# Optimization experiments

Hardware: AMD Instinct MI355X
Metric: run time of the kernel (lower is better)

The kernel has to match this reference:

```python
import jax, jax.numpy as jnp
import numpy as np

N, M = 1024, 1024
GATES = ["ii", "hi", "if", "hf", "ig", "hg", "io", "ho"]


def setup_inputs() -> dict:
    key = jax.random.key(0)
    names = ["x", "h", "c"] + [f"{p}_{g}" for g in GATES for p in ("L", "R", "b")]
    keys = jax.random.split(key, len(names))
    out = {}
    for nm, k in zip(names, keys):
        if nm in ("x", "h", "c"):
            sh = (N, M)
            scale = 1.0
        else:
            p = nm.split("_")[0]
            sh = {"L": (N, N), "R": (M, M), "b": (N, M)}[p]
            scale = 0.05  # keep gate pre-activations in a sane range
        out[nm] = jax.random.normal(k, sh, dtype=jnp.float32) * scale
    return out


def _klin(L, R, b, x):
    # kronecker_addmm: left @ x @ right + bias
    return L @ x @ R + b


def reference(x, h, c,
              L_ii, R_ii, b_ii, L_hi, R_hi, b_hi,
              L_if, R_if, b_if, L_hf, R_hf, b_hf,
              L_ig, R_ig, b_ig, L_hg, R_hg, b_hg,
              L_io, R_io, b_io, L_ho, R_ho, b_ho):
    i = jax.nn.sigmoid(_klin(L_ii, R_ii, b_ii, x) + _klin(L_hi, R_hi, b_hi, h))
    f = jax.nn.sigmoid(_klin(L_if, R_if, b_if, x) + _klin(L_hf, R_hf, b_hf, h))
    g = jnp.tanh(_klin(L_ig, R_ig, b_ig, x) + _klin(L_hg, R_hg, b_hg, h))
    o = jax.nn.sigmoid(_klin(L_io, R_io, b_io, x) + _klin(L_ho, R_ho, b_ho, h))
    c_new = f * c + i * g
    h_new = o * jnp.tanh(c_new)
    return (h_new, c_new)
```

## Files before the change

kernel.cpp:

```cpp
#include <hip/hip_runtime.h>
#include <stdint.h>

typedef __bf16 bf16x8 __attribute__((ext_vector_type(8)));
typedef float  f32x4  __attribute__((ext_vector_type(4)));
typedef uint16_t u16;

#define MAT_ELEMS (1024 * 1024)
#define LDK 1024


__device__ __forceinline__ u16 to_bf16(float f) {
  union { float f; uint32_t u; } v; v.f = f;
  uint32_t u = v.u;
  uint32_t r = u + 0x7FFFu + ((u >> 16) & 1u);
  return (u16)(r >> 16);
}

__device__ __forceinline__ float bf16_to_f32(u16 b) {
  union { uint32_t u; float f; } v; v.u = ((uint32_t)b) << 16;
  return v.f;
}

__device__ __forceinline__ void gll16(const void* g, void* l) {
  __builtin_amdgcn_global_load_lds(
      (__attribute__((address_space(1))) void*)const_cast<void*>(g),
      (__attribute__((address_space(3))) void*)(l),
      16, 0, 0);
}

__device__ __forceinline__ void wait_barrier() {
  asm volatile("s_waitcnt vmcnt(0)" ::: "memory");
  __builtin_amdgcn_s_barrier();
  __builtin_amdgcn_sched_barrier(0);
}

__device__ __forceinline__ float fast_sigmoid(float x) {
  x = fminf(fmaxf(x, -30.f), 30.f);
  return 1.0f / (1.0f + __expf(-x));
}

__device__ __forceinline__ float fast_tanh(float x) {
  x = fminf(fmaxf(x, -15.f), 15.f);
  float e = __expf(2.0f * x);
  return (e - 1.0f) / (e + 1.0f);
}


struct P8  { const float* p[8]; };
struct P10 { const float* p[10]; };
struct B8  { const float* b[8]; };

__global__ __launch_bounds__(256) void cast8_kernel(P8 s, u16* __restrict__ dst) {
  const float* src = s.p[blockIdx.y];
  u16* d = dst + ((size_t)blockIdx.y << 20);
  int i = (blockIdx.x * 256 + threadIdx.x) * 4;
  f32x4 v = *reinterpret_cast<const f32x4*>(src + i);
  ushort4 o;
  o.x = to_bf16(v[0]); o.y = to_bf16(v[1]);
  o.z = to_bf16(v[2]); o.w = to_bf16(v[3]);
  *reinterpret_cast<ushort4*>(d + i) = o;
}

__global__ __launch_bounds__(256) void transpose_cast_kernel(P10 s, u16* __restrict__ dstbase) {
  __shared__ float tile[32][65];
  const float* src = s.p[blockIdx.z];
  u16* dst = dstbase + ((size_t)blockIdx.z << 20);
  int c0 = blockIdx.x * 64;
  int r0 = blockIdx.y * 32;
  int cl = threadIdx.x & 63;
  int rg = threadIdx.x >> 6;
#pragma unroll
  for (int i = 0; i < 8; ++i) {
    int r = rg + i * 4;
    tile[r][cl] = src[(size_t)(r0 + r) * 1024 + c0 + cl];
  }
  __syncthreads();
  int kl = threadIdx.x & 31;
  int ng = threadIdx.x >> 5;
#pragma unroll
  for (int i = 0; i < 8; ++i) {
    int n = ng + i * 8;
    dst[(size_t)(c0 + n) * 1024 + r0 + kl] = to_bf16(tile[kl][n]);
  }
}


struct GemmCtx {
  const u16* A; const u16* B;
  int row0, col0;
  int tid, wr, wc, r16, kg, sw;
};

__device__ __forceinline__ void stage_tile(const GemmCtx& c, u16* As, u16* Bs, int kt) {
  int rho = c.tid >> 2;
  int sig = c.tid & 3;
  int swc = (sig ^ ((c.tid >> 3) & 3)) * 8;
  int kcol = kt * 32 + swc;
  gll16(c.A + (size_t)(c.row0 + rho) * LDK + kcol, As + c.tid * 8);
  gll16(c.B + (size_t)(c.col0 + rho) * LDK + kcol, Bs + c.tid * 8);
  gll16(c.B + (size_t)(c.col0 + rho + 128) * LDK + kcol, Bs + c.tid * 8 + 4096);
}

__device__ __forceinline__ void compute_tile(const GemmCtx& c, const u16* As,
                                             const u16* Bs, f32x4 acc[4][4]) {
  bf16x8 af[4], bfr[4];
#pragma unroll
  for (int n = 0; n < 4; ++n) {
    int Rb = c.wc * 64 + n * 16 + c.r16;
    bfr[n] = *reinterpret_cast<const bf16x8*>(Bs + Rb * 32 + ((c.kg ^ c.sw) * 8));
  }
#pragma unroll
  for (int m = 0; m < 4; ++m) {
    int Ra = c.wr * 64 + m * 16 + c.r16;
    af[m] = *reinterpret_cast<const bf16x8*>(As + Ra * 32 + ((c.kg ^ c.sw) * 8));
  }
#pragma unroll
  for (int m = 0; m < 4; ++m)
#pragma unroll
    for (int n = 0; n < 4; ++n)
      acc[m][n] = __builtin_amdgcn_mfma_f32_16x16x32_bf16(af[m], bfr[n], acc[m][n], 0, 0, 0);
}

__device__ __forceinline__ void gemm_body(
    const u16* __restrict__ A, const u16* __restrict__ B,
    int row0, int col0, u16* __restrict__ out,
    u16* As0, u16* Bs0, u16* As1, u16* Bs1)
{
  GemmCtx c;
  c.A = A; c.B = B; c.row0 = row0; c.col0 = col0;
  c.tid = threadIdx.x;
  int lane = c.tid & 63;
  int w = c.tid >> 6;
  c.wr  = w >> 2;
  c.wc  = w & 3;
  c.r16 = lane & 15;
  c.kg  = lane >> 4;
  c.sw  = (c.r16 >> 1) & 3;

  f32x4 acc[4][4];
#pragma unroll
  for (int m = 0; m < 4; ++m)
#pragma unroll
    for (int n = 0; n < 4; ++n) {
      f32x4 z = {0.f, 0.f, 0.f, 0.f};
      acc[m][n] = z;
    }

  stage_tile(c, As0, Bs0, 0);
  wait_barrier();

  for (int kt = 0; kt < 32; kt += 2) {
    stage_tile(c, As1, Bs1, kt + 1);
    compute_tile(c, As0, Bs0, acc);
    wait_barrier();
    if (kt + 2 < 32) stage_tile(c, As0, Bs0, kt + 2);
    compute_tile(c, As1, Bs1, acc);
    wait_barrier();
  }

#pragma unroll
  for (int m = 0; m < 4; ++m) {
#pragma unroll
    for (int r = 0; r < 4; ++r) {
      int row = row0 + c.wr * 64 + m * 16 + c.kg * 4 + r;
#pragma unroll
      for (int n = 0; n < 4; ++n) {
        int col = col0 + c.wc * 64 + n * 16 + c.r16;
        out[(size_t)row * 1024 + col] = to_bf16(acc[m][n][r]);
      }
    }
  }
}

__device__ __forceinline__ void swz_decode(int bx, int& g, int& row0, int& col0) {
  int wg = ((bx & 7) << 5) | (bx >> 3);
  g = wg >> 5;
  int t = wg & 31;
  row0 = (t >> 2) * 128;
  col0 = (t & 3) * 256;
}

__global__ __launch_bounds__(512) void gemm_stage1_kernel(
    const u16* __restrict__ Lb, const u16* __restrict__ xT,
    const u16* __restrict__ hT, u16* __restrict__ Tbuf)
{
  __shared__ u16 As0[128 * 32], Bs0[256 * 32];
  __shared__ u16 As1[128 * 32], Bs1[256 * 32];
  int g, row0, col0;
  swz_decode(blockIdx.x, g, row0, col0);
  const u16* A = Lb + ((size_t)g << 20);
  const u16* B = (g & 1) ? hT : xT;
  gemm_body(A, B, row0, col0, Tbuf + ((size_t)g << 20), As0, Bs0, As1, Bs1);
}

__global__ __launch_bounds__(512) void gemm_stage2_kernel(
    const u16* __restrict__ Tbuf, const u16* __restrict__ RT,
    u16* __restrict__ P)
{
  __shared__ u16 As0[128 * 32], Bs0[256 * 32];
  __shared__ u16 As1[128 * 32], Bs1[256 * 32];
  int g, row0, col0;
  swz_decode(blockIdx.x, g, row0, col0);
  const u16* A = Tbuf + ((size_t)g << 20);
  const u16* B = RT   + ((size_t)g << 20);
  gemm_body(A, B, row0, col0, P + ((size_t)g << 20), As0, Bs0, As1, Bs1);
}

__global__ __launch_bounds__(256) void lstm_cell_kernel(
    const u16* __restrict__ P, B8 bp, const float* __restrict__ c,
    float* __restrict__ out)
{
  int i = (blockIdx.x * 256 + threadIdx.x) * 4;
  ushort4 pv[8];
#pragma unroll
  for (int g = 0; g < 8; ++g)
    pv[g] = *reinterpret_cast<const ushort4*>(P + (size_t)g * MAT_ELEMS + i);
  f32x4 bv[8];
#pragma unroll
  for (int g = 0; g < 8; ++g)
    bv[g] = *reinterpret_cast<const f32x4*>(bp.b[g] + i);
  f32x4 cc = *reinterpret_cast<const f32x4*>(c + i);
  f32x4 hn, cn;
#pragma unroll
  for (int j = 0; j < 4; ++j) {
    float pi = bf16_to_f32((&pv[0].x)[j]) + bf16_to_f32((&pv[1].x)[j]) + bv[0][j] + bv[1][j];
    float pf = bf16_to_f32((&pv[2].x)[j]) + bf16_to_f32((&pv[3].x)[j]) + bv[2][j] + bv[3][j];
    float pg = bf16_to_f32((&pv[4].x)[j]) + bf16_to_f32((&pv[5].x)[j]) + bv[4][j] + bv[5][j];
    float po = bf16_to_f32((&pv[6].x)[j]) + bf16_to_f32((&pv[7].x)[j]) + bv[6][j] + bv[7][j];
    float ig = fast_sigmoid(pi);
    float fg = fast_sigmoid(pf);
    float gg = fast_tanh(pg);
    float og = fast_sigmoid(po);
    float cv = fg * cc[j] + ig * gg;
    cn[j] = cv;
    hn[j] = og * fast_tanh(cv);
  }
  *reinterpret_cast<f32x4*>(out + i) = hn;
  *reinterpret_cast<f32x4*>(out + MAT_ELEMS + i) = cn;
}


extern "C" void kernel_launch(void* const* d_in, const int* in_sizes, int n_in,
                              void* d_out, int out_size, void* d_ws, size_t ws_size,
                              hipStream_t stream) {
  const float* x = (const float*)d_in[0];
  const float* h = (const float*)d_in[1];
  const float* c = (const float*)d_in[2];

  u16* Lb   = (u16*)d_ws;
  u16* xT   = Lb + ((size_t)8 << 20);
  u16* hT   = xT + ((size_t)1 << 20);
  u16* RT   = hT + ((size_t)1 << 20);
  u16* Tbuf = RT + ((size_t)8 << 20);
  u16* P    = Tbuf + ((size_t)8 << 20);

  P8 lp;
  for (int g = 0; g < 8; ++g) lp.p[g] = (const float*)d_in[3 + 3 * g];
  P10 tp;
  tp.p[0] = x; tp.p[1] = h;
  for (int g = 0; g < 8; ++g) tp.p[2 + g] = (const float*)d_in[4 + 3 * g];
  B8 bp;
  for (int g = 0; g < 8; ++g) bp.b[g] = (const float*)d_in[5 + 3 * g];

  cast8_kernel<<<dim3(1024, 8), 256, 0, stream>>>(lp, Lb);
  transpose_cast_kernel<<<dim3(16, 32, 10), 256, 0, stream>>>(tp, xT);
  gemm_stage1_kernel<<<256, 512, 0, stream>>>(Lb, xT, hT, Tbuf);
  gemm_stage2_kernel<<<256, 512, 0, stream>>>(Tbuf, RT, P);
  lstm_cell_kernel<<<1024, 256, 0, stream>>>(P, bp, c, (float*)d_out);
}
```

Before: 242.3 us.

## Retile GEMMs to 128x128 blocks with BK=64 and 4 waves per block

Both GEMM stages change from 128x256 tiles with 8 waves and a K-step of 32 to 128x128 tiles with 4 waves and a K-step of 64. The LDS swizzle is rewritten as an 8-slot XOR pattern. The grid doubles to 512 blocks, which suits a GPU with 256 CUs better and halves the number of barriers in the K loop. In exchange, each block reuses less data, so global loads per output rise, and more LDS is used per block.

```diff
diff --git a/kernel.cpp b/kernel.cpp
--- a/kernel.cpp
+++ b/kernel.cpp
@@ -88,37 +88,48 @@
 struct GemmCtx {
   const u16* A; const u16* B;
   int row0, col0;
-  int tid, wr, wc, r16, kg, sw;
+  int tid, wr, wc, r16, kg;
 };
 
+__device__ __forceinline__ void stage_op(const u16* __restrict__ src, int base_row,
+                                         u16* lds, int kt, int tid) {
+  int r = tid >> 3;
+  int slot = (tid & 7) ^ (r & 7);
+  int kcol = kt * 64 + slot * 8;
+#pragma unroll
+  for (int i = 0; i < 4; ++i)
+    gll16(src + (size_t)(base_row + i * 32 + r) * LDK + kcol,
+          lds + i * 2048 + tid * 8);
+}
+
 __device__ __forceinline__ void stage_tile(const GemmCtx& c, u16* As, u16* Bs, int kt) {
-  int rho = c.tid >> 2;
-  int sig = c.tid & 3;
-  int swc = (sig ^ ((c.tid >> 3) & 3)) * 8;
-  int kcol = kt * 32 + swc;
-  gll16(c.A + (size_t)(c.row0 + rho) * LDK + kcol, As + c.tid * 8);
-  gll16(c.B + (size_t)(c.col0 + rho) * LDK + kcol, Bs + c.tid * 8);
-  gll16(c.B + (size_t)(c.col0 + rho + 128) * LDK + kcol, Bs + c.tid * 8 + 4096);
+  stage_op(c.A, c.row0, As, kt, c.tid);
+  stage_op(c.B, c.col0, Bs, kt, c.tid);
 }
 
 __device__ __forceinline__ void compute_tile(const GemmCtx& c, const u16* As,
                                              const u16* Bs, f32x4 acc[4][4]) {
-  bf16x8 af[4], bfr[4];
-#pragma unroll
-  for (int n = 0; n < 4; ++n) {
-    int Rb = c.wc * 64 + n * 16 + c.r16;
-    bfr[n] = *reinterpret_cast<const bf16x8*>(Bs + Rb * 32 + ((c.kg ^ c.sw) * 8));
-  }
-#pragma unroll
-  for (int m = 0; m < 4; ++m) {
-    int Ra = c.wr * 64 + m * 16 + c.r16;
-    af[m] = *reinterpret_cast<const bf16x8*>(As + Ra * 32 + ((c.kg ^ c.sw) * 8));
-  }
-#pragma unroll
-  for (int m = 0; m < 4; ++m)
-#pragma unroll
-    for (int n = 0; n < 4; ++n)
-      acc[m][n] = __builtin_amdgcn_mfma_f32_16x16x32_bf16(af[m], bfr[n], acc[m][n], 0, 0, 0);
+#pragma unroll
+  for (int ks = 0; ks < 2; ++ks) {
+    bf16x8 af[4], bfr[4];
+#pragma unroll
+    for (int m = 0; m < 4; ++m) {
+      int Ra = c.wr * 64 + m * 16 + c.r16;
+      int slot = (ks * 4 + c.kg) ^ (Ra & 7);
+      af[m] = *reinterpret_cast<const bf16x8*>(As + Ra * 64 + slot * 8);
+    }
+#pragma unroll
+    for (int n = 0; n < 4; ++n) {
+      int Rb = c.wc * 64 + n * 16 + c.r16;
+      int slot = (ks * 4 + c.kg) ^ (Rb & 7);
+      bfr[n] = *reinterpret_cast<const bf16x8*>(Bs + Rb * 64 + slot * 8);
+    }
+#pragma unroll
+    for (int m = 0; m < 4; ++m)
+#pragma unroll
+      for (int n = 0; n < 4; ++n)
+        acc[m][n] = __builtin_amdgcn_mfma_f32_16x16x32_bf16(af[m], bfr[n], acc[m][n], 0, 0, 0);
+  }
 }
 
 __device__ __forceinline__ void gemm_body(
@@ -131,11 +142,10 @@
   c.tid = threadIdx.x;
   int lane = c.tid & 63;
   int w = c.tid >> 6;
-  c.wr  = w >> 2;
-  c.wc  = w & 3;
+  c.wr  = w >> 1;
+  c.wc  = w & 1;
   c.r16 = lane & 15;
   c.kg  = lane >> 4;
-  c.sw  = (c.r16 >> 1) & 3;
 
   f32x4 acc[4][4];
 #pragma unroll
@@ -149,11 +159,11 @@
   stage_tile(c, As0, Bs0, 0);
   wait_barrier();
 
-  for (int kt = 0; kt < 32; kt += 2) {
+  for (int kt = 0; kt < 16; kt += 2) {
     stage_tile(c, As1, Bs1, kt + 1);
     compute_tile(c, As0, Bs0, acc);
     wait_barrier();
-    if (kt + 2 < 32) stage_tile(c, As0, Bs0, kt + 2);
+    if (kt + 2 < 16) stage_tile(c, As0, Bs0, kt + 2);
     compute_tile(c, As1, Bs1, acc);
     wait_barrier();
   }
@@ -173,19 +183,19 @@
 }
 
 __device__ __forceinline__ void swz_decode(int bx, int& g, int& row0, int& col0) {
-  int wg = ((bx & 7) << 5) | (bx >> 3);
-  g = wg >> 5;
-  int t = wg & 31;
-  row0 = (t >> 2) * 128;
-  col0 = (t & 3) * 256;
-}
-
-__global__ __launch_bounds__(512) void gemm_stage1_kernel(
+  int wg = ((bx & 7) << 6) | (bx >> 3);
+  g = wg >> 6;
+  int t = wg & 63;
+  row0 = (t >> 3) * 128;
+  col0 = (t & 7) * 128;
+}
+
+__global__ __launch_bounds__(256) void gemm_stage1_kernel(
     const u16* __restrict__ Lb, const u16* __restrict__ xT,
     const u16* __restrict__ hT, u16* __restrict__ Tbuf)
 {
-  __shared__ u16 As0[128 * 32], Bs0[256 * 32];
-  __shared__ u16 As1[128 * 32], Bs1[256 * 32];
+  __shared__ u16 As0[128 * 64], Bs0[128 * 64];
+  __shared__ u16 As1[128 * 64], Bs1[128 * 64];
   int g, row0, col0;
   swz_decode(blockIdx.x, g, row0, col0);
   const u16* A = Lb + ((size_t)g << 20);
@@ -193,12 +203,12 @@
   gemm_body(A, B, row0, col0, Tbuf + ((size_t)g << 20), As0, Bs0, As1, Bs1);
 }
 
-__global__ __launch_bounds__(512) void gemm_stage2_kernel(
+__global__ __launch_bounds__(256) void gemm_stage2_kernel(
     const u16* __restrict__ Tbuf, const u16* __restrict__ RT,
     u16* __restrict__ P)
 {
-  __shared__ u16 As0[128 * 32], Bs0[256 * 32];
-  __shared__ u16 As1[128 * 32], Bs1[256 * 32];
+  __shared__ u16 As0[128 * 64], Bs0[128 * 64];
+  __shared__ u16 As1[128 * 64], Bs1[128 * 64];
   int g, row0, col0;
   swz_decode(blockIdx.x, g, row0, col0);
   const u16* A = Tbuf + ((size_t)g << 20);
@@ -264,7 +274,7 @@
 
   cast8_kernel<<<dim3(1024, 8), 256, 0, stream>>>(lp, Lb);
   transpose_cast_kernel<<<dim3(16, 32, 10), 256, 0, stream>>>(tp, xT);
-  gemm_stage1_kernel<<<256, 512, 0, stream>>>(Lb, xT, hT, Tbuf);
-  gemm_stage2_kernel<<<256, 512, 0, stream>>>(Tbuf, RT, P);
+  gemm_stage1_kernel<<<512, 256, 0, stream>>>(Lb, xT, hT, Tbuf);
+  gemm_stage2_kernel<<<512, 256, 0, stream>>>(Tbuf, RT, P);
   lstm_cell_kernel<<<1024, 256, 0, stream>>>(P, bp, c, (float*)d_out);
 }
```

Result: faster. 232.9 us (-3.9%).
